# Optimization experiments

Hardware: AMD Instinct MI355X
Metric: run time of the kernel (lower is better)

## Reference

```python
import jax, jax.numpy as jnp
import numpy as np
from jax import lax

ALPHA_LO = float(np.exp(-1.0 / 5.0))
ALPHA_HI = float(np.exp(-1.0 / 25.0))
THRESHOLD = 1.0


def setup_inputs() -> dict:
    key = jax.random.key(0)
    k1, k2, k3, k4, k5 = jax.random.split(key, 5)
    B, T, I, H = 64, 1024, 512, 512
    x = jax.random.normal(k1, (B, T, I), dtype=jnp.float32)
    # kaiming-uniform-like small init for Linear weight
    bound = 1.0 / np.sqrt(I)
    W = jax.random.uniform(k2, (H, I), minval=-bound, maxval=bound, dtype=jnp.float32)
    alpha = ALPHA_LO + jax.random.uniform(k3, (H,), dtype=jnp.float32) * (ALPHA_HI - ALPHA_LO)
    u0 = jax.random.uniform(k4, (B, H), dtype=jnp.float32)
    s0 = jax.random.uniform(k5, (B, H), dtype=jnp.float32)
    return {"x": x, "W": W, "alpha": alpha, "u0": u0, "s0": s0}


def reference(x, W, alpha, u0, s0):
    # x: [B, T, I], W: [H, I] (torch Linear layout), alpha/u0/s0 over H
    al = jnp.clip(alpha, ALPHA_LO, ALPHA_HI)  # [H]
    Wx = jnp.einsum('bti,hi->bth', x, W)      # [B, T, H]

    def step(carry, wx_t):
        u, s = carry
        u = al * (u - s) + (1.0 - al) * wx_t
        s = (u - THRESHOLD > 0).astype(wx_t.dtype)
        return (u, s), s

    _, spikes = lax.scan(step, (u0, s0), jnp.swapaxes(Wx, 0, 1))  # [T, B, H]
    return jnp.swapaxes(spikes, 0, 1)  # [B, T, H]
```

## Files before the change

kernel.cpp:

```cpp
#include <hip/hip_runtime.h>


#define ALPHA_LO_F ((float)0.8187307530779818)
#define ALPHA_HI_F ((float)0.9607894391523232)

typedef float v4f __attribute__((ext_vector_type(4)));

#define TM 128
#define TN 128
#define TK 16
__global__ __launch_bounds__(256) void gemm_nt_f32(
    const float* __restrict__ A,
    const float* __restrict__ B,
    float* __restrict__ C,
    int M, int N, int K)
{
    __shared__ float As[TK][TM];
    __shared__ float Bs[TK][TN];

    const int tid = threadIdx.x;
    const int m0  = blockIdx.y * TM;
    const int n0  = blockIdx.x * TN;

    const int lrow = tid >> 1;
    const int lkq  = (tid & 1) * 8;

    const int tm = tid >> 4;
    const int tn = tid & 15;

    float acc[8][8] = {};

    const float* Arow = A + (size_t)(m0 + lrow) * K + lkq;
    const float* Brow = B + (size_t)(n0 + lrow) * K + lkq;

    for (int k0 = 0; k0 < K; k0 += TK) {
        float4 av0 = *(const float4*)(Arow + k0);
        float4 av1 = *(const float4*)(Arow + k0 + 4);
        float4 bv0 = *(const float4*)(Brow + k0);
        float4 bv1 = *(const float4*)(Brow + k0 + 4);
        As[lkq + 0][lrow] = av0.x;  As[lkq + 1][lrow] = av0.y;
        As[lkq + 2][lrow] = av0.z;  As[lkq + 3][lrow] = av0.w;
        As[lkq + 4][lrow] = av1.x;  As[lkq + 5][lrow] = av1.y;
        As[lkq + 6][lrow] = av1.z;  As[lkq + 7][lrow] = av1.w;
        Bs[lkq + 0][lrow] = bv0.x;  Bs[lkq + 1][lrow] = bv0.y;
        Bs[lkq + 2][lrow] = bv0.z;  Bs[lkq + 3][lrow] = bv0.w;
        Bs[lkq + 4][lrow] = bv1.x;  Bs[lkq + 5][lrow] = bv1.y;
        Bs[lkq + 6][lrow] = bv1.z;  Bs[lkq + 7][lrow] = bv1.w;
        __syncthreads();

        #pragma unroll
        for (int k = 0; k < TK; ++k) {
            const float* Ak  = &As[k][tm * 8];
            const float* Bk0 = &Bs[k][tn * 4];
            const float* Bk1 = &Bs[k][64 + tn * 4];
            float4 a0 = *(const float4*)(Ak);
            float4 a1 = *(const float4*)(Ak + 4);
            float4 b0 = *(const float4*)(Bk0);
            float4 b1 = *(const float4*)(Bk1);
            float a[8]  = {a0.x, a0.y, a0.z, a0.w, a1.x, a1.y, a1.z, a1.w};
            float bv[8] = {b0.x, b0.y, b0.z, b0.w, b1.x, b1.y, b1.z, b1.w};
            #pragma unroll
            for (int i = 0; i < 8; ++i) {
                #pragma unroll
                for (int j = 0; j < 8; ++j)
                    acc[i][j] = __builtin_fmaf(a[i], bv[j], acc[i][j]);
            }
        }
        __syncthreads();
    }

    #pragma unroll
    for (int i = 0; i < 8; ++i) {
        float* Crow = C + (size_t)(m0 + tm * 8 + i) * N + n0;
        v4f v0, v1;
        v0.x = acc[i][0]; v0.y = acc[i][1]; v0.z = acc[i][2]; v0.w = acc[i][3];
        v1.x = acc[i][4]; v1.y = acc[i][5]; v1.z = acc[i][6]; v1.w = acc[i][7];
        __builtin_nontemporal_store(v0, (v4f*)(Crow + tn * 4));
        __builtin_nontemporal_store(v1, (v4f*)(Crow + 64 + tn * 4));
    }
}

#define C_T  64
#define NBUF 4

__global__ __launch_bounds__(320) void lif_scan(
    float* __restrict__ buf,
    const float* __restrict__ alpha,
    const float* __restrict__ u0,
    const float* __restrict__ s0,
    int B, int T, int H)
{
    __shared__ float S[NBUF][C_T][64];

    const int tid  = threadIdx.x;
    const int wid  = tid >> 6;
    const int lane = tid & 63;
    const int b    = blockIdx.y;
    const int h0   = blockIdx.x * 64;
    const int nch  = T / C_T;

    float* base = buf + (size_t)b * T * H + h0;

    if (wid == 0) {
        const int h = h0 + lane;
        float al = alpha[h];
        al = fminf(fmaxf(al, ALPHA_LO_F), ALPHA_HI_F);
        const float oma = 1.0f - al;
        float u = u0[(size_t)b * H + h];
        float s = s0[(size_t)b * H + h];

        for (int j = 0; j < nch; ++j) {
            asm volatile("s_barrier" ::: "memory");
            const float* Sj = &S[j & (NBUF - 1)][0][0] + lane;
            float* orow = base + (size_t)j * C_T * H + lane;
            for (int tb = 0; tb < C_T; tb += 16) {
                float w[16];
                #pragma unroll
                for (int tt = 0; tt < 16; ++tt)
                    w[tt] = Sj[(tb + tt) * 64];
                #pragma unroll
                for (int tt = 0; tt < 16; ++tt) {
                    u = al * (u - s) + oma * w[tt];
                    s = (u - 1.0f > 0.0f) ? 1.0f : 0.0f;
                    w[tt] = s;
                }
                #pragma unroll
                for (int tt = 0; tt < 16; ++tt)
                    __builtin_nontemporal_store(w[tt], &orow[(size_t)(tb + tt) * H]);
            }
            asm volatile("s_waitcnt lgkmcnt(0)" ::: "memory");
            asm volatile("s_barrier" ::: "memory");
        }
    } else {
        const int lw = wid - 1;

        #define ISSUE_CHUNK(c)                                                  \
            {                                                                   \
                const int cc = (c);                                             \
                char* sb = (char*)&S[cc & (NBUF - 1)][0][0];                    \
                _Pragma("unroll")                                               \
                for (int q = 0; q < 4; ++q) {                                   \
                    const int i = lw + 4 * q;                                   \
                    const int t = cc * C_T + i * 4 + (lane >> 4);               \
                    const float* g = base + (size_t)t * H + (lane & 15) * 4;    \
                    __builtin_amdgcn_global_load_lds(                           \
                        (const __attribute__((address_space(1))) unsigned int*)g, \
                        (__attribute__((address_space(3))) unsigned int*)(sb + i * 1024), \
                        16, 0, 0);                                              \
                }                                                               \
            }

        for (int c = 0; c < NBUF - 1; ++c) ISSUE_CHUNK(c)

        for (int j = 0; j < nch; ++j) {
            const int c = j + NBUF - 1;
            if (c < nch) ISSUE_CHUNK(c)
            if (j < nch - 3)       asm volatile("s_waitcnt vmcnt(12)" ::: "memory");
            else if (j == nch - 3) asm volatile("s_waitcnt vmcnt(8)"  ::: "memory");
            else if (j == nch - 2) asm volatile("s_waitcnt vmcnt(4)"  ::: "memory");
            else                   asm volatile("s_waitcnt vmcnt(0)"  ::: "memory");
            asm volatile("s_barrier" ::: "memory");
            asm volatile("s_barrier" ::: "memory");
        }
        #undef ISSUE_CHUNK
    }
}

extern "C" void kernel_launch(void* const* d_in, const int* in_sizes, int n_in,
                              void* d_out, int out_size, void* d_ws, size_t ws_size,
                              hipStream_t stream) {
    const float* x     = (const float*)d_in[0];
    const float* W     = (const float*)d_in[1];
    const float* alpha = (const float*)d_in[2];
    const float* u0    = (const float*)d_in[3];
    const float* s0    = (const float*)d_in[4];
    float* out = (float*)d_out;

    const int H = in_sizes[2];
    const int I = in_sizes[1] / H;
    const int B = in_sizes[3] / H;
    const int T = in_sizes[0] / (B * I);
    const int M = B * T;

    dim3 grid1(H / TN, M / TM);
    gemm_nt_f32<<<grid1, 256, 0, stream>>>(x, W, out, M, H, I);

    dim3 grid2(H / 64, B);
    lif_scan<<<grid2, 320, 0, stream>>>(out, alpha, u0, s0, B, T, H);
}
```

Measured before the change: 606.9 us.

## Write GEMM output in H-blocked workspace layout for contiguous scan loads

The GEMM epilogue now writes Wx into a workspace laid out as [B][H/64][T][64], so each scan block's input is one contiguous stream. The scan kernel then reads contiguous 1 KB rows instead of 256-byte strided segments and writes spikes to the separate output buffer. The aim is more efficient DRAM access in the bandwidth-bound scan. The cost is an extra 128 MB workspace buffer, a division in the GEMM store addressing, and a fallback to the old in-place path when the workspace is too small.

```diff
diff --git a/kernel.cpp b/kernel.cpp
--- a/kernel.cpp
+++ b/kernel.cpp
@@ -9,11 +9,12 @@
 #define TM 128
 #define TN 128
 #define TK 16
+template <int BLK>
 __global__ __launch_bounds__(256) void gemm_nt_f32(
     const float* __restrict__ A,
     const float* __restrict__ B,
     float* __restrict__ C,
-    int M, int N, int K)
+    int M, int N, int K, int T)
 {
     __shared__ float As[TK][TM];
     __shared__ float Bs[TK][TN];
@@ -69,21 +70,118 @@
         __syncthreads();
     }
 
+    const int NS = N >> 6;
     #pragma unroll
     for (int i = 0; i < 8; ++i) {
-        float* Crow = C + (size_t)(m0 + tm * 8 + i) * N + n0;
+        const int row = m0 + tm * 8 + i;
         v4f v0, v1;
         v0.x = acc[i][0]; v0.y = acc[i][1]; v0.z = acc[i][2]; v0.w = acc[i][3];
         v1.x = acc[i][4]; v1.y = acc[i][5]; v1.z = acc[i][6]; v1.w = acc[i][7];
-        __builtin_nontemporal_store(v0, (v4f*)(Crow + tn * 4));
-        __builtin_nontemporal_store(v1, (v4f*)(Crow + 64 + tn * 4));
+        if constexpr (BLK) {
+            const int b = row / T, t = row - b * T;
+            const int c0 = n0 + tn * 4, c1 = n0 + 64 + tn * 4;
+            float* p0 = C + (((size_t)b * NS + (c0 >> 6)) * T + t) * 64 + (c0 & 63);
+            float* p1 = C + (((size_t)b * NS + (c1 >> 6)) * T + t) * 64 + (c1 & 63);
+            __builtin_nontemporal_store(v0, (v4f*)p0);
+            __builtin_nontemporal_store(v1, (v4f*)p1);
+        } else {
+            float* Crow = C + (size_t)row * N + n0;
+            __builtin_nontemporal_store(v0, (v4f*)(Crow + tn * 4));
+            __builtin_nontemporal_store(v1, (v4f*)(Crow + 64 + tn * 4));
+        }
     }
 }
 
 #define C_T  64
 #define NBUF 4
 
-__global__ __launch_bounds__(320) void lif_scan(
+__global__ __launch_bounds__(320) void lif_scan_blk(
+    const float* __restrict__ ws,
+    float* __restrict__ out,
+    const float* __restrict__ alpha,
+    const float* __restrict__ u0,
+    const float* __restrict__ s0,
+    int B, int T, int H)
+{
+    __shared__ float S[NBUF][C_T][64];
+
+    const int tid  = threadIdx.x;
+    const int wid  = tid >> 6;
+    const int lane = tid & 63;
+    const int b    = blockIdx.y;
+    const int sidx = blockIdx.x;
+    const int h0   = sidx * 64;
+    const int NS   = H >> 6;
+    const int nch  = T / C_T;
+
+    const float* src = ws + ((size_t)b * NS + sidx) * T * 64;
+
+    if (wid == 0) {
+        const int h = h0 + lane;
+        float al = alpha[h];
+        al = fminf(fmaxf(al, ALPHA_LO_F), ALPHA_HI_F);
+        const float oma = 1.0f - al;
+        float u = u0[(size_t)b * H + h];
+        float s = s0[(size_t)b * H + h];
+
+        for (int j = 0; j < nch; ++j) {
+            asm volatile("s_barrier" ::: "memory");
+            const float* Sj = &S[j & (NBUF - 1)][0][0] + lane;
+            float* orow = out + ((size_t)b * T + j * C_T) * H + h;
+            for (int tb = 0; tb < C_T; tb += 16) {
+                float w[16];
+                #pragma unroll
+                for (int tt = 0; tt < 16; ++tt)
+                    w[tt] = Sj[(tb + tt) * 64];
+                #pragma unroll
+                for (int tt = 0; tt < 16; ++tt) {
+                    u = al * (u - s) + oma * w[tt];
+                    s = (u - 1.0f > 0.0f) ? 1.0f : 0.0f;
+                    w[tt] = s;
+                }
+                #pragma unroll
+                for (int tt = 0; tt < 16; ++tt)
+                    __builtin_nontemporal_store(w[tt], orow + (size_t)(tb + tt) * H);
+            }
+            asm volatile("s_waitcnt lgkmcnt(0)" ::: "memory");
+            asm volatile("s_barrier" ::: "memory");
+        }
+    } else {
+        const int lw = wid - 1;
+
+        #define ISSUE_CHUNK(c)                                                  \
+            {                                                                   \
+                const int cc = (c);                                             \
+                char* sb = (char*)&S[cc & (NBUF - 1)][0][0];                    \
+                const float* gc = src + (size_t)cc * C_T * 64;                  \
+                _Pragma("unroll")                                               \
+                for (int q = 0; q < 4; ++q) {                                   \
+                    const int i = lw + 4 * q;                                   \
+                    const float* g = gc + i * 256 + lane * 4;                   \
+                    __builtin_amdgcn_global_load_lds(                           \
+                        (const __attribute__((address_space(1))) unsigned int*)g, \
+                        (__attribute__((address_space(3))) unsigned int*)(sb + i * 1024), \
+                        16, 0, 0);                                              \
+                }                                                               \
+            }
+
+        for (int c = 0; c < NBUF - 1; ++c) ISSUE_CHUNK(c)
+
+        for (int j = 0; j < nch; ++j) {
+            const int c = j + NBUF - 1;
+            if (c < nch) ISSUE_CHUNK(c)
+            if (j < nch - 3)       asm volatile("s_waitcnt vmcnt(12)" ::: "memory");
+            else if (j == nch - 3) asm volatile("s_waitcnt vmcnt(8)"  ::: "memory");
+            else if (j == nch - 2) asm volatile("s_waitcnt vmcnt(4)"  ::: "memory");
+            else                   asm volatile("s_waitcnt vmcnt(0)"  ::: "memory");
+            asm volatile("s_barrier" ::: "memory");
+            asm volatile("s_barrier" ::: "memory");
+        }
+        #undef ISSUE_CHUNK
+    }
+}
+
+__global__ __launch_bounds__(320) void lif_scan_ip(
     float* __restrict__ buf,
     const float* __restrict__ alpha,
     const float* __restrict__ u0,
@@ -182,9 +280,18 @@
     const int T = in_sizes[0] / (B * I);
     const int M = B * T;
 
+    const size_t need = (size_t)M * H * sizeof(float);
+    const bool blocked = (ws_size >= need) && ((H & 63) == 0) && (d_ws != nullptr);
+
     dim3 grid1(H / TN, M / TM);
-    gemm_nt_f32<<<grid1, 256, 0, stream>>>(x, W, out, M, H, I);
-
     dim3 grid2(H / 64, B);
-    lif_scan<<<grid2, 320, 0, stream>>>(out, alpha, u0, s0, B, T, H);
-}
+
+    if (blocked) {
+        float* ws = (float*)d_ws;
+        gemm_nt_f32<1><<<grid1, 256, 0, stream>>>(x, W, ws, M, H, I, T);
+        lif_scan_blk<<<grid2, 320, 0, stream>>>(ws, out, alpha, u0, s0, B, T, H);
+    } else {
+        gemm_nt_f32<0><<<grid1, 256, 0, stream>>>(x, W, out, M, H, I, T);
+        lif_scan_ip<<<grid2, 320, 0, stream>>>(out, alpha, u0, s0, B, T, H);
+    }
+}
```

Result: slower. 627.9 us (+3.5%).

## Replace LDS-pipelined LIF scan with one-block-per-batch register-prefetch scan

Applied to the files above, without the earlier changes.

Adds a scan kernel that runs one block per batch row with one thread per hidden unit. Each thread double-buffers 32 timesteps in registers and writes spikes in place. This removes the producer/consumer wave split, the LDS staging and the barriers of the previous scan. In exchange it launches only B blocks, which can leave many CUs idle and reduces memory-level parallelism.

```diff
diff --git a/kernel.cpp b/kernel.cpp
--- a/kernel.cpp
+++ b/kernel.cpp
@@ -80,10 +80,62 @@
     }
 }
 
+#define SPF 32
+__global__ __launch_bounds__(1024) void lif_scan_wide(
+    float* __restrict__ buf,
+    const float* __restrict__ alpha,
+    const float* __restrict__ u0,
+    const float* __restrict__ s0,
+    int B, int T, int H)
+{
+    const int h = threadIdx.x;
+    const int b = blockIdx.x;
+    if (h >= H) return;
+
+    float al = alpha[h];
+    al = fminf(fmaxf(al, ALPHA_LO_F), ALPHA_HI_F);
+    const float oma = 1.0f - al;
+
+    float u = u0[(size_t)b * H + h];
+    float s = s0[(size_t)b * H + h];
+
+    const size_t sH = (size_t)H;
+    size_t idx = (size_t)b * T * H + h;
+
+    float cur[SPF], nxt[SPF];
+    #pragma unroll
+    for (int j = 0; j < SPF; ++j) cur[j] = buf[idx + (size_t)j * sH];
+
+    for (int t0 = 0; t0 + SPF <= T; t0 += SPF) {
+        const size_t nidx = idx + (size_t)SPF * sH;
+        if (t0 + SPF < T) {
+            #pragma unroll
+            for (int j = 0; j < SPF; ++j) nxt[j] = buf[nidx + (size_t)j * sH];
+        }
+        #pragma unroll
+        for (int j = 0; j < SPF; ++j) {
+            u = al * (u - s) + oma * cur[j];
+            s = (u - 1.0f > 0.0f) ? 1.0f : 0.0f;
+            cur[j] = s;
+        }
+        #pragma unroll
+        for (int j = 0; j < SPF; ++j)
+            __builtin_nontemporal_store(cur[j], &buf[idx + (size_t)j * sH]);
+        #pragma unroll
+        for (int j = 0; j < SPF; ++j) cur[j] = nxt[j];
+        idx = nidx;
+    }
+    for (int t = (T / SPF) * SPF; t < T; ++t) {
+        float w = buf[(size_t)b * T * H + (size_t)t * H + h];
+        u = al * (u - s) + oma * w;
+        s = (u - 1.0f > 0.0f) ? 1.0f : 0.0f;
+        __builtin_nontemporal_store(s, &buf[(size_t)b * T * H + (size_t)t * H + h]);
+    }
+}
+
 #define C_T  64
 #define NBUF 4
-
-__global__ __launch_bounds__(320) void lif_scan(
+__global__ __launch_bounds__(320) void lif_scan_ip(
     float* __restrict__ buf,
     const float* __restrict__ alpha,
     const float* __restrict__ u0,
@@ -185,6 +237,10 @@
     dim3 grid1(H / TN, M / TM);
     gemm_nt_f32<<<grid1, 256, 0, stream>>>(x, W, out, M, H, I);
 
-    dim3 grid2(H / 64, B);
-    lif_scan<<<grid2, 320, 0, stream>>>(out, alpha, u0, s0, B, T, H);
-}
+    if (H <= 1024 && (H & 63) == 0 && T >= SPF) {
+        lif_scan_wide<<<B, H, 0, stream>>>(out, alpha, u0, s0, B, T, H);
+    } else {
+        dim3 grid2(H / 64, B);
+        lif_scan_ip<<<grid2, 320, 0, stream>>>(out, alpha, u0, s0, B, T, H);
+    }
+}
```

Result: slower. 882.6 us (+45.4%).
